# Optimization experiments

Measured on AMD Instinct MI355X. Metric: run time of the kernel, lower is better.

The kernel has to match this reference:

```python
import jax, jax.numpy as jnp
import numpy as np

B, S, HID = 4, 2048, 1024
NH, IM, E = 4, 2048, 4
EPS = 1e-6


def setup_inputs() -> dict:
    key = jax.random.key(0)
    ks = jax.random.split(key, 12)
    init = lambda k, shape: (jax.random.normal(k, shape, jnp.float32) * 0.02)
    return {
        "hidden_states": jax.random.normal(ks[0], (B, S, HID), jnp.float32),
        "ln1_w": jnp.ones((HID,), jnp.float32),
        "wq": init(ks[1], (HID, HID)),
        "wk": init(ks[2], (HID, HID)),
        "wv": init(ks[3], (HID, HID)),
        "wo": init(ks[4], (HID, HID)),
        "ln2_w": jnp.ones((HID,), jnp.float32),
        "router_w": init(ks[5], (HID, E)),
        "router_b": jnp.zeros((E,), jnp.float32),
        "gate_w": init(ks[6], (E, HID, IM)),
        "up_w": init(ks[7], (E, HID, IM)),
        "down_w": init(ks[8], (E, IM, HID)),
    }


def _rms(x, w):
    return w * (x * jax.lax.rsqrt(jnp.mean(x * x, axis=-1, keepdims=True) + EPS))


def reference(hidden_states, ln1_w, wq, wk, wv, wo, ln2_w,
              router_w, router_b, gate_w, up_w, down_w):
    b, s, h = hidden_states.shape
    nh, d = NH, h // NH

    # ---- attention block (elu+1 feature map, then full softmax) ----
    x = _rms(hidden_states, ln1_w)
    q = (x @ wq).reshape(b, s, nh, d).transpose(0, 2, 1, 3)  # [b,nh,s,d]
    k = (x @ wk).reshape(b, s, nh, d).transpose(0, 2, 1, 3)
    v = (x @ wv).reshape(b, s, nh, d).transpose(0, 2, 1, 3)
    q = jax.nn.elu(q) + 1.0
    k = jax.nn.elu(k) + 1.0
    scores = jnp.einsum('bhqd,bhkd->bhqk', q, k)
    attn = jax.nn.softmax(scores, axis=-1)  # dropout is identity at eval
    o = jnp.einsum('bhqk,bhkd->bhqd', attn, v)
    o = o.transpose(0, 2, 1, 3).reshape(b, s, h) @ wo
    h1 = hidden_states + o

    # ---- MoE block: router softmax, balance loss, dense expert loop ----
    x2 = _rms(h1, ln2_w)
    logits = x2 @ router_w + router_b            # [b,s,E]
    rw = jax.nn.softmax(logits, axis=-1)
    mean_routing = rw.mean(axis=0)               # mean over batch dim only, [s,E]
    balance_loss = jnp.mean((mean_routing - 1.0 / E) ** 2) * 0.01

    # source computes EVERY expert over all tokens, weighted by the FULL
    # softmax routing weight (top-k weights are computed but unused)
    moe_out = jnp.zeros_like(x2)
    for i in range(E):
        g = jax.nn.silu(x2 @ gate_w[i])
        u = x2 @ up_w[i]
        moe_out = moe_out + ((g * u) @ down_w[i]) * rw[..., i:i + 1]

    return h1 + moe_out, balance_loss
```

## Files before the change

kernel.cpp:

```cpp
#include <hip/hip_runtime.h>
#include <cstdint>
#include <cstddef>

#define B_    4
#define S_    2048
#define HID_  1024
#define NH_   4
#define HD_   256
#define IM_   2048
#define E_    4
#define M_    8192
#define NHG_  4

typedef __bf16 bf16x8 __attribute__((ext_vector_type(8)));
typedef float  f32x4  __attribute__((ext_vector_type(4)));

__device__ __forceinline__ unsigned short f32_to_bf16(float f) {
  unsigned int u = __float_as_uint(f);
  u += 0x7fffu + ((u >> 16) & 1u);
  return (unsigned short)(u >> 16);
}
__device__ __forceinline__ float bf16_to_f32(unsigned short s) {
  return __uint_as_float((unsigned int)s << 16);
}

__device__ __forceinline__ void gload16(const unsigned short* g, unsigned short* l) {
  __builtin_amdgcn_global_load_lds(
      (const __attribute__((address_space(1))) void*)g,
      (__attribute__((address_space(3))) void*)l, 16, 0, 0);
}

__device__ __forceinline__ void swizzle_xy(int& bx, int& by) {
  const int gx = gridDim.x, gy = gridDim.y;
  const int flat = blockIdx.x + blockIdx.y * gx;
  const int xcd = flat & 7, i = flat >> 3;
  const int rpx = gy >> 3;
  bx = i % gx;
  by = xcd * rpx + i / gx;
}

#define EPI_F32      0
#define EPI_ELU_BF16 1
#define EPI_VT       2
#define EPI_PV_O     3
#define EPI_WO       4
#define EPI_DOWN     5

struct EpiAux {
  float* c_f32;
  unsigned short* c_bf16;
  const float* add_src;
  float* out2;
  const float* rw;
  int expert;
  long long strideCz;
  int ldc;
};

template<int EPI>
__global__ __launch_bounds__(256) void gemm_bf16k(
    const unsigned short* __restrict__ A, int lda, long long sAo, long long sAi, int zbA,
    const unsigned short* __restrict__ B, int ldb, long long sBo, long long sBi, int zbB,
    int zshift, int zmask, int zbC, int K, EpiAux aux)
{
  __shared__ unsigned short As[2][128 * 32];
  __shared__ unsigned short Bs[2][128 * 32];

  const int t = threadIdx.x;
  int bx, by;
  swizzle_xy(bx, by);
  const int m0 = by * 128, n0 = bx * 128;
  const int z  = blockIdx.z;
  const int zA = z + zbA, zB = z + zbB, zC = z + zbC;
  const unsigned short* Ab = A + (long long)(zA >> zshift) * sAo + (long long)(zA & zmask) * sAi;
  const unsigned short* Bb = B + (long long)(zB >> zshift) * sBo + (long long)(zB & zmask) * sBi;

  const int lane = t & 63, wave = t >> 6;
  const int wm = (wave >> 1) * 64, wn = (wave & 1) * 64;
  const int lrow = lane & 15, quad = lane >> 4;

  f32x4 acc[4][4] = {};

  const int srow = lane >> 2;
  const int sko  = (lane & 3) * 8;
  const unsigned short* aRow0 = Ab + (long long)(m0 + wave * 16       + srow) * lda + sko;
  const unsigned short* aRow1 = Ab + (long long)(m0 + (wave + 4) * 16 + srow) * lda + sko;
  const unsigned short* bRow0 = Bb + (long long)(n0 + wave * 16       + srow) * ldb + sko;
  const unsigned short* bRow1 = Bb + (long long)(n0 + (wave + 4) * 16 + srow) * ldb + sko;
  const int dst0 = (wave * 16) * 32, dst1 = ((wave + 4) * 16) * 32;

  gload16(aRow0, &As[0][dst0]);
  gload16(aRow1, &As[0][dst1]);
  gload16(bRow0, &Bs[0][dst0]);
  gload16(bRow1, &Bs[0][dst1]);

  int cur = 0;
  for (int kk = 0; kk < K; kk += 32, cur ^= 1) {
    __syncthreads();
    if (kk + 32 < K) {
      const int nxt = cur ^ 1, k2 = kk + 32;
      gload16(aRow0 + k2, &As[nxt][dst0]);
      gload16(aRow1 + k2, &As[nxt][dst1]);
      gload16(bRow0 + k2, &Bs[nxt][dst0]);
      gload16(bRow1 + k2, &Bs[nxt][dst1]);
    }
    bf16x8 af[4], bfr[4];
    #pragma unroll
    for (int i = 0; i < 4; ++i) {
      af[i]  = *reinterpret_cast<const bf16x8*>(&As[cur][(wm + i * 16 + lrow) * 32 + quad * 8]);
      bfr[i] = *reinterpret_cast<const bf16x8*>(&Bs[cur][(wn + i * 16 + lrow) * 32 + quad * 8]);
    }
    #pragma unroll
    for (int i = 0; i < 4; ++i)
      #pragma unroll
      for (int j = 0; j < 4; ++j)
        acc[i][j] = __builtin_amdgcn_mfma_f32_16x16x32_bf16(af[i], bfr[j], acc[i][j], 0, 0, 0);
  }

  #pragma unroll
  for (int mi = 0; mi < 4; ++mi) {
    #pragma unroll
    for (int ni = 0; ni < 4; ++ni) {
      #pragma unroll
      for (int r = 0; r < 4; ++r) {
        const int gm = m0 + wm + mi * 16 + quad * 4 + r;
        const int gn = n0 + wn + ni * 16 + lrow;
        const float val = acc[mi][ni][r];
        if (EPI == EPI_F32) {
          aux.c_f32[(long long)zC * aux.strideCz + (long long)gm * aux.ldc + gn] = val;
        } else if (EPI == EPI_ELU_BF16) {
          const float e = val > 0.f ? val + 1.f : __expf(val);
          aux.c_bf16[(long long)gm * aux.ldc + gn] = f32_to_bf16(e);
        } else if (EPI == EPI_VT) {
          const int b = gm >> 11, s = gm & (S_ - 1);
          const int h = gn >> 8, d = gn & (HD_ - 1);
          aux.c_bf16[((long long)(b * NH_ + h) * HD_ + d) * S_ + s] = f32_to_bf16(val);
        } else if (EPI == EPI_PV_O) {
          const int b = zC >> 2, h = zC & (NH_ - 1);
          aux.c_bf16[((long long)(b * S_ + gm)) * HID_ + h * HD_ + gn] = f32_to_bf16(val);
        } else if (EPI == EPI_WO) {
          const long long idx = (long long)gm * HID_ + gn;
          aux.out2[idx] = val + aux.add_src[idx];
        } else if (EPI == EPI_DOWN) {
          const long long idx = (long long)gm * HID_ + gn;
          aux.out2[idx] += val * aux.rw[(long long)gm * E_ + aux.expert];
        }
      }
    }
  }
}

__global__ __launch_bounds__(256, 2) void gemm_gu_k(
    const unsigned short* __restrict__ A,
    const unsigned short* __restrict__ Bg,
    const unsigned short* __restrict__ Bu,
    unsigned short* __restrict__ gu)
{
  __shared__ unsigned short As[2][128 * 32];
  __shared__ unsigned short Bgs[2][128 * 32];
  __shared__ unsigned short Bus[2][128 * 32];

  const int t = threadIdx.x;
  int bx, by;
  swizzle_xy(bx, by);
  const int m0 = by * 128, n0 = bx * 128;

  const int lane = t & 63, wave = t >> 6;
  const int wm = (wave >> 1) * 64, wn = (wave & 1) * 64;
  const int lrow = lane & 15, quad = lane >> 4;

  f32x4 accg[4][4] = {}, accu[4][4] = {};

  const int srow = lane >> 2;
  const int sko  = (lane & 3) * 8;
  const unsigned short* aRow0 = A  + (long long)(m0 + wave * 16       + srow) * HID_ + sko;
  const unsigned short* aRow1 = A  + (long long)(m0 + (wave + 4) * 16 + srow) * HID_ + sko;
  const unsigned short* gRow0 = Bg + (long long)(n0 + wave * 16       + srow) * HID_ + sko;
  const unsigned short* gRow1 = Bg + (long long)(n0 + (wave + 4) * 16 + srow) * HID_ + sko;
  const unsigned short* uRow0 = Bu + (long long)(n0 + wave * 16       + srow) * HID_ + sko;
  const unsigned short* uRow1 = Bu + (long long)(n0 + (wave + 4) * 16 + srow) * HID_ + sko;
  const int dst0 = (wave * 16) * 32, dst1 = ((wave + 4) * 16) * 32;

  gload16(aRow0, &As[0][dst0]);
  gload16(aRow1, &As[0][dst1]);
  gload16(gRow0, &Bgs[0][dst0]);
  gload16(gRow1, &Bgs[0][dst1]);
  gload16(uRow0, &Bus[0][dst0]);
  gload16(uRow1, &Bus[0][dst1]);

  int cur = 0;
  for (int kk = 0; kk < HID_; kk += 32, cur ^= 1) {
    __syncthreads();
    if (kk + 32 < HID_) {
      const int nxt = cur ^ 1, k2 = kk + 32;
      gload16(aRow0 + k2, &As[nxt][dst0]);
      gload16(aRow1 + k2, &As[nxt][dst1]);
      gload16(gRow0 + k2, &Bgs[nxt][dst0]);
      gload16(gRow1 + k2, &Bgs[nxt][dst1]);
      gload16(uRow0 + k2, &Bus[nxt][dst0]);
      gload16(uRow1 + k2, &Bus[nxt][dst1]);
    }
    bf16x8 af[4], bg[4], bu[4];
    #pragma unroll
    for (int i = 0; i < 4; ++i) {
      af[i] = *reinterpret_cast<const bf16x8*>(&As[cur][(wm + i * 16 + lrow) * 32 + quad * 8]);
      bg[i] = *reinterpret_cast<const bf16x8*>(&Bgs[cur][(wn + i * 16 + lrow) * 32 + quad * 8]);
      bu[i] = *reinterpret_cast<const bf16x8*>(&Bus[cur][(wn + i * 16 + lrow) * 32 + quad * 8]);
    }
    #pragma unroll
    for (int i = 0; i < 4; ++i)
      #pragma unroll
      for (int j = 0; j < 4; ++j) {
        accg[i][j] = __builtin_amdgcn_mfma_f32_16x16x32_bf16(af[i], bg[j], accg[i][j], 0, 0, 0);
        accu[i][j] = __builtin_amdgcn_mfma_f32_16x16x32_bf16(af[i], bu[j], accu[i][j], 0, 0, 0);
      }
  }

  #pragma unroll
  for (int mi = 0; mi < 4; ++mi)
    #pragma unroll
    for (int ni = 0; ni < 4; ++ni)
      #pragma unroll
      for (int r = 0; r < 4; ++r) {
        const int gm = m0 + wm + mi * 16 + quad * 4 + r;
        const int gn = n0 + wn + ni * 16 + lrow;
        const float g = accg[mi][ni][r];
        const float u = accu[mi][ni][r];
        const float sg = g / (1.f + __expf(-g));
        gu[(long long)gm * IM_ + gn] = f32_to_bf16(sg * u);
      }
}

__global__ void transpose_cast_k(const float* __restrict__ in,
                                 unsigned short* __restrict__ out, int R, int C)
{
  __shared__ float tile[32][33];
  const long long bo = (long long)blockIdx.z * R * C;
  const int c0 = blockIdx.x * 32, r0 = blockIdx.y * 32;
  const int tx = threadIdx.x, ty = threadIdx.y;
  #pragma unroll
  for (int i = 0; i < 32; i += 8)
    tile[ty + i][tx] = in[bo + (long long)(r0 + ty + i) * C + c0 + tx];
  __syncthreads();
  #pragma unroll
  for (int i = 0; i < 32; i += 8)
    out[bo + (long long)(c0 + ty + i) * R + r0 + tx] = f32_to_bf16(tile[tx][ty + i]);
}

__global__ __launch_bounds__(256) void rmsnorm_cast_k(
    const float* __restrict__ x, const float* __restrict__ w,
    unsigned short* __restrict__ out)
{
  __shared__ float red[4];
  const int row = blockIdx.x, t = threadIdx.x;
  const float4 v = reinterpret_cast<const float4*>(x + (long long)row * HID_)[t];
  float ss = v.x * v.x + v.y * v.y + v.z * v.z + v.w * v.w;
  #pragma unroll
  for (int off = 32; off > 0; off >>= 1) ss += __shfl_down(ss, off, 64);
  if ((t & 63) == 0) red[t >> 6] = ss;
  __syncthreads();
  ss = red[0] + red[1] + red[2] + red[3];
  const float inv = rsqrtf(ss * (1.0f / HID_) + 1e-6f);
  const float4 wv = reinterpret_cast<const float4*>(w)[t];
  ushort4 o;
  o.x = f32_to_bf16(v.x * inv * wv.x);
  o.y = f32_to_bf16(v.y * inv * wv.y);
  o.z = f32_to_bf16(v.z * inv * wv.z);
  o.w = f32_to_bf16(v.w * inv * wv.w);
  reinterpret_cast<ushort4*>(out + (long long)row * HID_)[t] = o;
}

__global__ __launch_bounds__(256) void softmax_rows_k(float* __restrict__ scores)
{
  __shared__ float red[4];
  const long long rbase = ((long long)blockIdx.y * S_ + blockIdx.x) * S_;
  float* row = scores + rbase;
  const int t = threadIdx.x;
  float v[8];
  #pragma unroll
  for (int i = 0; i < 8; ++i) v[i] = row[t + i * 256];
  float m = v[0];
  #pragma unroll
  for (int i = 1; i < 8; ++i) m = fmaxf(m, v[i]);
  #pragma unroll
  for (int off = 32; off > 0; off >>= 1) m = fmaxf(m, __shfl_down(m, off, 64));
  if ((t & 63) == 0) red[t >> 6] = m;
  __syncthreads();
  m = fmaxf(fmaxf(red[0], red[1]), fmaxf(red[2], red[3]));
  __syncthreads();
  float s = 0.f;
  #pragma unroll
  for (int i = 0; i < 8; ++i) { v[i] = __expf(v[i] - m); s += v[i]; }
  #pragma unroll
  for (int off = 32; off > 0; off >>= 1) s += __shfl_down(s, off, 64);
  if ((t & 63) == 0) red[t >> 6] = s;
  __syncthreads();
  const float inv = 1.0f / (red[0] + red[1] + red[2] + red[3]);
  unsigned short* prow = reinterpret_cast<unsigned short*>(scores) + rbase * 2;
  #pragma unroll
  for (int i = 0; i < 8; ++i) prow[t + i * 256] = f32_to_bf16(v[i] * inv);
}

__global__ __launch_bounds__(256) void router_k(
    const float* __restrict__ h1, const float* __restrict__ ln2w,
    const float* __restrict__ rwgt, const float* __restrict__ rbias,
    float* __restrict__ rw)
{
  const int wv = threadIdx.x >> 6, lane = threadIdx.x & 63;
  const long long m = (long long)blockIdx.x * 4 + wv;
  const float* xr = h1 + m * HID_;
  float xv[16];
  float ss = 0.f;
  #pragma unroll
  for (int i = 0; i < 16; ++i) { xv[i] = xr[lane + i * 64]; ss += xv[i] * xv[i]; }
  #pragma unroll
  for (int off = 32; off > 0; off >>= 1) ss += __shfl_down(ss, off, 64);
  ss = __shfl(ss, 0, 64);
  const float inv = rsqrtf(ss * (1.0f / HID_) + 1e-6f);
  float l0 = 0, l1 = 0, l2 = 0, l3 = 0;
  #pragma unroll
  for (int i = 0; i < 16; ++i) {
    const int k = lane + i * 64;
    const float xn = xv[i] * inv * ln2w[k];
    const float4 wr = reinterpret_cast<const float4*>(rwgt)[k];
    l0 += xn * wr.x; l1 += xn * wr.y; l2 += xn * wr.z; l3 += xn * wr.w;
  }
  #pragma unroll
  for (int off = 32; off > 0; off >>= 1) {
    l0 += __shfl_down(l0, off, 64);
    l1 += __shfl_down(l1, off, 64);
    l2 += __shfl_down(l2, off, 64);
    l3 += __shfl_down(l3, off, 64);
  }
  if (lane == 0) {
    l0 += rbias[0]; l1 += rbias[1]; l2 += rbias[2]; l3 += rbias[3];
    const float mx = fmaxf(fmaxf(l0, l1), fmaxf(l2, l3));
    const float e0 = __expf(l0 - mx), e1 = __expf(l1 - mx);
    const float e2 = __expf(l2 - mx), e3 = __expf(l3 - mx);
    const float is = 1.0f / (e0 + e1 + e2 + e3);
    reinterpret_cast<float4*>(rw)[m] = make_float4(e0 * is, e1 * is, e2 * is, e3 * is);
  }
}

__global__ __launch_bounds__(256) void balance_k(const float* __restrict__ rw,
                                                 float* __restrict__ out_scalar)
{
  __shared__ float red[4];
  float acc = 0.f;
  for (int it = threadIdx.x; it < S_ * E_; it += 256) {
    const int s = it >> 2, e = it & 3;
    float mr = 0.f;
    #pragma unroll
    for (int b = 0; b < B_; ++b) mr += rw[((long long)b * S_ + s) * E_ + e];
    mr *= (1.0f / B_);
    const float d = mr - 1.0f / E_;
    acc += d * d;
  }
  #pragma unroll
  for (int off = 32; off > 0; off >>= 1) acc += __shfl_down(acc, off, 64);
  if ((threadIdx.x & 63) == 0) red[threadIdx.x >> 6] = acc;
  __syncthreads();
  if (threadIdx.x == 0)
    out_scalar[0] = (red[0] + red[1] + red[2] + red[3]) * (0.01f / (S_ * E_));
}

extern "C" void kernel_launch(void* const* d_in, const int* in_sizes, int n_in,
                              void* d_out, int out_size, void* d_ws, size_t ws_size,
                              hipStream_t stream)
{
  const float* hidden   = (const float*)d_in[0];
  const float* ln1w     = (const float*)d_in[1];
  const float* wq       = (const float*)d_in[2];
  const float* wk       = (const float*)d_in[3];
  const float* wv       = (const float*)d_in[4];
  const float* wo       = (const float*)d_in[5];
  const float* ln2w     = (const float*)d_in[6];
  const float* router_w = (const float*)d_in[7];
  const float* router_b = (const float*)d_in[8];
  const float* gate_w   = (const float*)d_in[9];
  const float* up_w     = (const float*)d_in[10];
  const float* down_w   = (const float*)d_in[11];
  float* out = (float*)d_out;

  char* ws = (char*)d_ws;
  size_t off = 0;
  auto carve = [&](size_t bytes) {
    off = (off + 255) & ~(size_t)255;
    char* p = ws + off;
    off += bytes;
    return p;
  };
  unsigned short* wqT   = (unsigned short*)carve((size_t)HID_ * HID_ * 2);
  unsigned short* wkT   = (unsigned short*)carve((size_t)HID_ * HID_ * 2);
  unsigned short* wvT   = (unsigned short*)carve((size_t)HID_ * HID_ * 2);
  unsigned short* woT   = (unsigned short*)carve((size_t)HID_ * HID_ * 2);
  unsigned short* x_bf  = (unsigned short*)carve((size_t)M_ * HID_ * 2);
  unsigned short* qb    = (unsigned short*)carve((size_t)M_ * HID_ * 2);
  unsigned short* kb    = (unsigned short*)carve((size_t)M_ * HID_ * 2);
  unsigned short* vT    = (unsigned short*)carve((size_t)M_ * HID_ * 2);
  float*          rwbuf = (float*)carve((size_t)M_ * E_ * 4);
  char*           ubase = carve((size_t)NHG_ * S_ * S_ * 4);
  float*          scores = (float*)ubase;
  unsigned short* gateT = (unsigned short*)(ubase);
  unsigned short* upT   = (unsigned short*)(ubase + (size_t)16 * 1024 * 1024);
  unsigned short* downT = (unsigned short*)(ubase + (size_t)32 * 1024 * 1024);
  unsigned short* o_bf  = x_bf;
  unsigned short* x2_bf = qb;
  unsigned short* gu    = kb;

  const dim3 blk256(256), blkT(32, 8);

  transpose_cast_k<<<dim3(32, 32, 1), blkT, 0, stream>>>(wq, wqT, HID_, HID_);
  transpose_cast_k<<<dim3(32, 32, 1), blkT, 0, stream>>>(wk, wkT, HID_, HID_);
  transpose_cast_k<<<dim3(32, 32, 1), blkT, 0, stream>>>(wv, wvT, HID_, HID_);
  transpose_cast_k<<<dim3(32, 32, 1), blkT, 0, stream>>>(wo, woT, HID_, HID_);

  rmsnorm_cast_k<<<M_, blk256, 0, stream>>>(hidden, ln1w, x_bf);

  {
    EpiAux a{}; a.c_bf16 = qb; a.ldc = HID_;
    gemm_bf16k<EPI_ELU_BF16><<<dim3(8, 64, 1), blk256, 0, stream>>>(
        x_bf, HID_, 0, 0, 0, wqT, HID_, 0, 0, 0, 0, 0, 0, HID_, a);
  }
  {
    EpiAux a{}; a.c_bf16 = kb; a.ldc = HID_;
    gemm_bf16k<EPI_ELU_BF16><<<dim3(8, 64, 1), blk256, 0, stream>>>(
        x_bf, HID_, 0, 0, 0, wkT, HID_, 0, 0, 0, 0, 0, 0, HID_, a);
  }
  {
    EpiAux a{}; a.c_bf16 = vT;
    gemm_bf16k<EPI_VT><<<dim3(8, 64, 1), blk256, 0, stream>>>(
        x_bf, HID_, 0, 0, 0, wvT, HID_, 0, 0, 0, 0, 0, 0, HID_, a);
  }

  for (int grp = 0; grp < 16 / NHG_; ++grp) {
    EpiAux as{}; as.c_f32 = scores; as.ldc = S_; as.strideCz = (long long)S_ * S_;
    gemm_bf16k<EPI_F32><<<dim3(16, 16, NHG_), blk256, 0, stream>>>(
        qb, HID_, (long long)S_ * HID_, HD_, grp * NHG_,
        kb, HID_, (long long)S_ * HID_, HD_, grp * NHG_,
        2, 3, 0, HD_, as);
    softmax_rows_k<<<dim3(S_, NHG_, 1), blk256, 0, stream>>>(scores);
    EpiAux ap{}; ap.c_bf16 = o_bf;
    gemm_bf16k<EPI_PV_O><<<dim3(2, 16, NHG_), blk256, 0, stream>>>(
        (const unsigned short*)scores, 2 * S_, (long long)S_ * 2 * S_, 0, 0,
        vT, S_, (long long)HD_ * S_, 0, grp * NHG_,
        0, 0, grp * NHG_, S_, ap);
  }

  transpose_cast_k<<<dim3(64, 32, E_), blkT, 0, stream>>>(gate_w, gateT, HID_, IM_);
  transpose_cast_k<<<dim3(64, 32, E_), blkT, 0, stream>>>(up_w,   upT,   HID_, IM_);
  transpose_cast_k<<<dim3(32, 64, E_), blkT, 0, stream>>>(down_w, downT, IM_, HID_);

  {
    EpiAux a{}; a.add_src = hidden; a.out2 = out;
    gemm_bf16k<EPI_WO><<<dim3(8, 64, 1), blk256, 0, stream>>>(
        o_bf, HID_, 0, 0, 0, woT, HID_, 0, 0, 0, 0, 0, 0, HID_, a);
  }

  rmsnorm_cast_k<<<M_, blk256, 0, stream>>>(out, ln2w, x2_bf);
  router_k<<<M_ / 4, blk256, 0, stream>>>(out, ln2w, router_w, router_b, rwbuf);
  balance_k<<<1, blk256, 0, stream>>>(rwbuf, out + (size_t)M_ * HID_);

  for (int i = 0; i < E_; ++i) {
    gemm_gu_k<<<dim3(16, 64, 1), blk256, 0, stream>>>(
        x2_bf, gateT + (size_t)i * IM_ * HID_, upT + (size_t)i * IM_ * HID_, gu);
    EpiAux ad{}; ad.out2 = out; ad.rw = rwbuf; ad.expert = i;
    gemm_bf16k<EPI_DOWN><<<dim3(8, 64, 1), blk256, 0, stream>>>(
        gu, IM_, 0, 0, 0, downT + (size_t)i * HID_ * IM_, IM_, 0, 0, 0,
        0, 0, 0, IM_, ad);
  }
}
```

Baseline: 1.195 ms.

## Pair MoE experts in gate/up and down GEMMs, fuse Q/K projections and transposes

Fuses the Q and K projections into one dual-output GEMM sharing the A tile. The routing weight now multiplies gu in the gate/up epilogue instead of the down epilogue. Two experts run per launch: gate/up over a z=2 grid into two gu buffers, then one down GEMM that accumulates both experts' K loops before a single read-modify-write of out. This halves the output RMW traffic and the launch count. The weight transposes are batched into fewer launches, at the cost of a larger workspace (extra gu buffer), higher LDS use in the down kernel, and a fallback path when the workspace is too small.

Result: slower. 1.390 ms (+16.4%).

```diff
diff --git a/kernel.cpp b/kernel.cpp
--- a/kernel.cpp
+++ b/kernel.cpp
@@ -20,9 +20,6 @@
   u += 0x7fffu + ((u >> 16) & 1u);
   return (unsigned short)(u >> 16);
 }
-__device__ __forceinline__ float bf16_to_f32(unsigned short s) {
-  return __uint_as_float((unsigned int)s << 16);
-}
 
 __device__ __forceinline__ void gload16(const unsigned short* g, unsigned short* l) {
   __builtin_amdgcn_global_load_lds(
@@ -40,7 +37,6 @@
 }
 
 #define EPI_F32      0
-#define EPI_ELU_BF16 1
 #define EPI_VT       2
 #define EPI_PV_O     3
 #define EPI_WO       4
@@ -51,8 +47,6 @@
   unsigned short* c_bf16;
   const float* add_src;
   float* out2;
-  const float* rw;
-  int expert;
   long long strideCz;
   int ldc;
 };
@@ -128,9 +122,6 @@
         const float val = acc[mi][ni][r];
         if (EPI == EPI_F32) {
           aux.c_f32[(long long)zC * aux.strideCz + (long long)gm * aux.ldc + gn] = val;
-        } else if (EPI == EPI_ELU_BF16) {
-          const float e = val > 0.f ? val + 1.f : __expf(val);
-          aux.c_bf16[(long long)gm * aux.ldc + gn] = f32_to_bf16(e);
         } else if (EPI == EPI_VT) {
           const int b = gm >> 11, s = gm & (S_ - 1);
           const int h = gn >> 8, d = gn & (HD_ - 1);
@@ -143,50 +134,59 @@
           aux.out2[idx] = val + aux.add_src[idx];
         } else if (EPI == EPI_DOWN) {
           const long long idx = (long long)gm * HID_ + gn;
-          aux.out2[idx] += val * aux.rw[(long long)gm * E_ + aux.expert];
+          aux.out2[idx] += val;
         }
       }
     }
   }
 }
 
-__global__ __launch_bounds__(256, 2) void gemm_gu_k(
+#define EPI2_QK 0
+#define EPI2_GU 1
+
+template<int EPI2>
+__global__ __launch_bounds__(256) void gemm_dual_k(
     const unsigned short* __restrict__ A,
-    const unsigned short* __restrict__ Bg,
-    const unsigned short* __restrict__ Bu,
-    unsigned short* __restrict__ gu)
+    const unsigned short* __restrict__ B0b,
+    const unsigned short* __restrict__ B1b,
+    long long sB, int zb,
+    unsigned short* __restrict__ out0, unsigned short* __restrict__ out1,
+    const float* __restrict__ rw)
 {
   __shared__ unsigned short As[2][128 * 32];
-  __shared__ unsigned short Bgs[2][128 * 32];
-  __shared__ unsigned short Bus[2][128 * 32];
+  __shared__ unsigned short B0s[2][128 * 32];
+  __shared__ unsigned short B1s[2][128 * 32];
 
   const int t = threadIdx.x;
   int bx, by;
   swizzle_xy(bx, by);
   const int m0 = by * 128, n0 = bx * 128;
+  const int z = blockIdx.z;
+  const unsigned short* Bb0 = B0b + (long long)z * sB;
+  const unsigned short* Bb1 = B1b + (long long)z * sB;
 
   const int lane = t & 63, wave = t >> 6;
   const int wm = (wave >> 1) * 64, wn = (wave & 1) * 64;
   const int lrow = lane & 15, quad = lane >> 4;
 
-  f32x4 accg[4][4] = {}, accu[4][4] = {};
+  f32x4 acc0[4][4] = {}, acc1[4][4] = {};
 
   const int srow = lane >> 2;
   const int sko  = (lane & 3) * 8;
-  const unsigned short* aRow0 = A  + (long long)(m0 + wave * 16       + srow) * HID_ + sko;
-  const unsigned short* aRow1 = A  + (long long)(m0 + (wave + 4) * 16 + srow) * HID_ + sko;
-  const unsigned short* gRow0 = Bg + (long long)(n0 + wave * 16       + srow) * HID_ + sko;
-  const unsigned short* gRow1 = Bg + (long long)(n0 + (wave + 4) * 16 + srow) * HID_ + sko;
-  const unsigned short* uRow0 = Bu + (long long)(n0 + wave * 16       + srow) * HID_ + sko;
-  const unsigned short* uRow1 = Bu + (long long)(n0 + (wave + 4) * 16 + srow) * HID_ + sko;
+  const unsigned short* aRow0 = A   + (long long)(m0 + wave * 16       + srow) * HID_ + sko;
+  const unsigned short* aRow1 = A   + (long long)(m0 + (wave + 4) * 16 + srow) * HID_ + sko;
+  const unsigned short* gRow0 = Bb0 + (long long)(n0 + wave * 16       + srow) * HID_ + sko;
+  const unsigned short* gRow1 = Bb0 + (long long)(n0 + (wave + 4) * 16 + srow) * HID_ + sko;
+  const unsigned short* uRow0 = Bb1 + (long long)(n0 + wave * 16       + srow) * HID_ + sko;
+  const unsigned short* uRow1 = Bb1 + (long long)(n0 + (wave + 4) * 16 + srow) * HID_ + sko;
   const int dst0 = (wave * 16) * 32, dst1 = ((wave + 4) * 16) * 32;
 
   gload16(aRow0, &As[0][dst0]);
   gload16(aRow1, &As[0][dst1]);
-  gload16(gRow0, &Bgs[0][dst0]);
-  gload16(gRow1, &Bgs[0][dst1]);
-  gload16(uRow0, &Bus[0][dst0]);
-  gload16(uRow1, &Bus[0][dst1]);
+  gload16(gRow0, &B0s[0][dst0]);
+  gload16(gRow1, &B0s[0][dst1]);
+  gload16(uRow0, &B1s[0][dst0]);
+  gload16(uRow1, &B1s[0][dst1]);
 
   int cur = 0;
   for (int kk = 0; kk < HID_; kk += 32, cur ^= 1) {
@@ -195,24 +195,127 @@
       const int nxt = cur ^ 1, k2 = kk + 32;
       gload16(aRow0 + k2, &As[nxt][dst0]);
       gload16(aRow1 + k2, &As[nxt][dst1]);
-      gload16(gRow0 + k2, &Bgs[nxt][dst0]);
-      gload16(gRow1 + k2, &Bgs[nxt][dst1]);
-      gload16(uRow0 + k2, &Bus[nxt][dst0]);
-      gload16(uRow1 + k2, &Bus[nxt][dst1]);
-    }
-    bf16x8 af[4], bg[4], bu[4];
+      gload16(gRow0 + k2, &B0s[nxt][dst0]);
+      gload16(gRow1 + k2, &B0s[nxt][dst1]);
+      gload16(uRow0 + k2, &B1s[nxt][dst0]);
+      gload16(uRow1 + k2, &B1s[nxt][dst1]);
+    }
+    bf16x8 af[4], b0[4], b1[4];
     #pragma unroll
     for (int i = 0; i < 4; ++i) {
       af[i] = *reinterpret_cast<const bf16x8*>(&As[cur][(wm + i * 16 + lrow) * 32 + quad * 8]);
-      bg[i] = *reinterpret_cast<const bf16x8*>(&Bgs[cur][(wn + i * 16 + lrow) * 32 + quad * 8]);
-      bu[i] = *reinterpret_cast<const bf16x8*>(&Bus[cur][(wn + i * 16 + lrow) * 32 + quad * 8]);
+      b0[i] = *reinterpret_cast<const bf16x8*>(&B0s[cur][(wn + i * 16 + lrow) * 32 + quad * 8]);
+      b1[i] = *reinterpret_cast<const bf16x8*>(&B1s[cur][(wn + i * 16 + lrow) * 32 + quad * 8]);
     }
     #pragma unroll
     for (int i = 0; i < 4; ++i)
       #pragma unroll
       for (int j = 0; j < 4; ++j) {
-        accg[i][j] = __builtin_amdgcn_mfma_f32_16x16x32_bf16(af[i], bg[j], accg[i][j], 0, 0, 0);
-        accu[i][j] = __builtin_amdgcn_mfma_f32_16x16x32_bf16(af[i], bu[j], accu[i][j], 0, 0, 0);
+        acc0[i][j] = __builtin_amdgcn_mfma_f32_16x16x32_bf16(af[i], b0[j], acc0[i][j], 0, 0, 0);
+        acc1[i][j] = __builtin_amdgcn_mfma_f32_16x16x32_bf16(af[i], b1[j], acc1[i][j], 0, 0, 0);
+      }
+  }
+
+  unsigned short* dsel = (z == 0) ? out0 : out1;
+  const int expert = zb + z;
+
+  #pragma unroll
+  for (int mi = 0; mi < 4; ++mi)
+    #pragma unroll
+    for (int r = 0; r < 4; ++r) {
+      const int gm = m0 + wm + mi * 16 + quad * 4 + r;
+      float rwv = 0.f;
+      if (EPI2 == EPI2_GU) rwv = rw[(long long)gm * E_ + expert];
+      #pragma unroll
+      for (int ni = 0; ni < 4; ++ni) {
+        const int gn = n0 + wn + ni * 16 + lrow;
+        const float v0 = acc0[mi][ni][r];
+        const float v1 = acc1[mi][ni][r];
+        if (EPI2 == EPI2_QK) {
+          const float eq = v0 > 0.f ? v0 + 1.f : __expf(v0);
+          const float ek = v1 > 0.f ? v1 + 1.f : __expf(v1);
+          out0[(long long)gm * HID_ + gn] = f32_to_bf16(eq);
+          out1[(long long)gm * HID_ + gn] = f32_to_bf16(ek);
+        } else {
+          const float sg = v0 / (1.f + __expf(-v0));
+          dsel[(long long)gm * IM_ + gn] = f32_to_bf16(sg * v1 * rwv);
+        }
+      }
+    }
+}
+
+__global__ __launch_bounds__(256) void gemm_down2_k(
+    const unsigned short* __restrict__ A0,
+    const unsigned short* __restrict__ A1,
+    const unsigned short* __restrict__ B0,
+    const unsigned short* __restrict__ B1,
+    float* __restrict__ out)
+{
+  __shared__ unsigned short A0s[2][128 * 32];
+  __shared__ unsigned short A1s[2][128 * 32];
+  __shared__ unsigned short B0s[2][128 * 32];
+  __shared__ unsigned short B1s[2][128 * 32];
+
+  const int t = threadIdx.x;
+  int bx, by;
+  swizzle_xy(bx, by);
+  const int m0 = by * 128, n0 = bx * 128;
+
+  const int lane = t & 63, wave = t >> 6;
+  const int wm = (wave >> 1) * 64, wn = (wave & 1) * 64;
+  const int lrow = lane & 15, quad = lane >> 4;
+
+  f32x4 acc[4][4] = {};
+
+  const int srow = lane >> 2;
+  const int sko  = (lane & 3) * 8;
+  const unsigned short* a0r0 = A0 + (long long)(m0 + wave * 16       + srow) * IM_ + sko;
+  const unsigned short* a0r1 = A0 + (long long)(m0 + (wave + 4) * 16 + srow) * IM_ + sko;
+  const unsigned short* a1r0 = A1 + (long long)(m0 + wave * 16       + srow) * IM_ + sko;
+  const unsigned short* a1r1 = A1 + (long long)(m0 + (wave + 4) * 16 + srow) * IM_ + sko;
+  const unsigned short* b0r0 = B0 + (long long)(n0 + wave * 16       + srow) * IM_ + sko;
+  const unsigned short* b0r1 = B0 + (long long)(n0 + (wave + 4) * 16 + srow) * IM_ + sko;
+  const unsigned short* b1r0 = B1 + (long long)(n0 + wave * 16       + srow) * IM_ + sko;
+  const unsigned short* b1r1 = B1 + (long long)(n0 + (wave + 4) * 16 + srow) * IM_ + sko;
+  const int dst0 = (wave * 16) * 32, dst1 = ((wave + 4) * 16) * 32;
+
+  gload16(a0r0, &A0s[0][dst0]);
+  gload16(a0r1, &A0s[0][dst1]);
+  gload16(a1r0, &A1s[0][dst0]);
+  gload16(a1r1, &A1s[0][dst1]);
+  gload16(b0r0, &B0s[0][dst0]);
+  gload16(b0r1, &B0s[0][dst1]);
+  gload16(b1r0, &B1s[0][dst0]);
+  gload16(b1r1, &B1s[0][dst1]);
+
+  int cur = 0;
+  for (int kk = 0; kk < IM_; kk += 32, cur ^= 1) {
+    __syncthreads();
+    if (kk + 32 < IM_) {
+      const int nxt = cur ^ 1, k2 = kk + 32;
+      gload16(a0r0 + k2, &A0s[nxt][dst0]);
+      gload16(a0r1 + k2, &A0s[nxt][dst1]);
+      gload16(a1r0 + k2, &A1s[nxt][dst0]);
+      gload16(a1r1 + k2, &A1s[nxt][dst1]);
+      gload16(b0r0 + k2, &B0s[nxt][dst0]);
+      gload16(b0r1 + k2, &B0s[nxt][dst1]);
+      gload16(b1r0 + k2, &B1s[nxt][dst0]);
+      gload16(b1r1 + k2, &B1s[nxt][dst1]);
+    }
+    bf16x8 a0f[4], a1f[4], b0f[4], b1f[4];
+    #pragma unroll
+    for (int i = 0; i < 4; ++i) {
+      a0f[i] = *reinterpret_cast<const bf16x8*>(&A0s[cur][(wm + i * 16 + lrow) * 32 + quad * 8]);
+      a1f[i] = *reinterpret_cast<const bf16x8*>(&A1s[cur][(wm + i * 16 + lrow) * 32 + quad * 8]);
+      b0f[i] = *reinterpret_cast<const bf16x8*>(&B0s[cur][(wn + i * 16 + lrow) * 32 + quad * 8]);
+      b1f[i] = *reinterpret_cast<const bf16x8*>(&B1s[cur][(wn + i * 16 + lrow) * 32 + quad * 8]);
+    }
+    #pragma unroll
+    for (int i = 0; i < 4; ++i)
+      #pragma unroll
+      for (int j = 0; j < 4; ++j) {
+        acc[i][j] = __builtin_amdgcn_mfma_f32_16x16x32_bf16(a0f[i], b0f[j], acc[i][j], 0, 0, 0);
+        acc[i][j] = __builtin_amdgcn_mfma_f32_16x16x32_bf16(a1f[i], b1f[j], acc[i][j], 0, 0, 0);
       }
   }
 
@@ -224,11 +327,49 @@
       for (int r = 0; r < 4; ++r) {
         const int gm = m0 + wm + mi * 16 + quad * 4 + r;
         const int gn = n0 + wn + ni * 16 + lrow;
-        const float g = accg[mi][ni][r];
-        const float u = accu[mi][ni][r];
-        const float sg = g / (1.f + __expf(-g));
-        gu[(long long)gm * IM_ + gn] = f32_to_bf16(sg * u);
+        out[(long long)gm * HID_ + gn] += acc[mi][ni][r];
       }
+}
+
+__global__ void transpose_cast4_k(const float* s0, const float* s1,
+                                  const float* s2, const float* s3,
+                                  unsigned short* __restrict__ out, int R, int C)
+{
+  __shared__ float tile[32][33];
+  const int z = blockIdx.z;
+  const float* in = (z == 0) ? s0 : (z == 1) ? s1 : (z == 2) ? s2 : s3;
+  unsigned short* o = out + (long long)z * R * C;
+  const int c0 = blockIdx.x * 32, r0 = blockIdx.y * 32;
+  const int tx = threadIdx.x, ty = threadIdx.y;
+  #pragma unroll
+  for (int i = 0; i < 32; i += 8)
+    tile[ty + i][tx] = in[(long long)(r0 + ty + i) * C + c0 + tx];
+  __syncthreads();
+  #pragma unroll
+  for (int i = 0; i < 32; i += 8)
+    o[(long long)(c0 + ty + i) * R + r0 + tx] = f32_to_bf16(tile[tx][ty + i]);
+}
+
+__global__ void transpose_cast2x4_k(const float* __restrict__ sA,
+                                    const float* __restrict__ sB,
+                                    unsigned short* __restrict__ dA,
+                                    unsigned short* __restrict__ dB,
+                                    int R, int C)
+{
+  __shared__ float tile[32][33];
+  const int z = blockIdx.z;
+  const long long eo = (long long)(z & 3) * R * C;
+  const float* in = ((z < 4) ? sA : sB) + eo;
+  unsigned short* o = ((z < 4) ? dA : dB) + eo;
+  const int c0 = blockIdx.x * 32, r0 = blockIdx.y * 32;
+  const int tx = threadIdx.x, ty = threadIdx.y;
+  #pragma unroll
+  for (int i = 0; i < 32; i += 8)
+    tile[ty + i][tx] = in[(long long)(r0 + ty + i) * C + c0 + tx];
+  __syncthreads();
+  #pragma unroll
+  for (int i = 0; i < 32; i += 8)
+    o[(long long)(c0 + ty + i) * R + r0 + tx] = f32_to_bf16(tile[tx][ty + i]);
 }
 
 __global__ void transpose_cast_k(const float* __restrict__ in,
@@ -400,33 +541,26 @@
   unsigned short* vT    = (unsigned short*)carve((size_t)M_ * HID_ * 2);
   float*          rwbuf = (float*)carve((size_t)M_ * E_ * 4);
   char*           ubase = carve((size_t)NHG_ * S_ * S_ * 4);
+  const size_t base_bytes = off;
   float*          scores = (float*)ubase;
   unsigned short* gateT = (unsigned short*)(ubase);
   unsigned short* upT   = (unsigned short*)(ubase + (size_t)16 * 1024 * 1024);
   unsigned short* downT = (unsigned short*)(ubase + (size_t)32 * 1024 * 1024);
   unsigned short* o_bf  = x_bf;
   unsigned short* x2_bf = qb;
-  unsigned short* gu    = kb;
+  unsigned short* gu0   = kb;
+  unsigned short* gu1   = (unsigned short*)carve((size_t)M_ * IM_ * 2);
+  const bool paired = (ws_size >= off);
+  (void)base_bytes;
 
   const dim3 blk256(256), blkT(32, 8);
 
-  transpose_cast_k<<<dim3(32, 32, 1), blkT, 0, stream>>>(wq, wqT, HID_, HID_);
-  transpose_cast_k<<<dim3(32, 32, 1), blkT, 0, stream>>>(wk, wkT, HID_, HID_);
-  transpose_cast_k<<<dim3(32, 32, 1), blkT, 0, stream>>>(wv, wvT, HID_, HID_);
-  transpose_cast_k<<<dim3(32, 32, 1), blkT, 0, stream>>>(wo, woT, HID_, HID_);
+  transpose_cast4_k<<<dim3(32, 32, 4), blkT, 0, stream>>>(wq, wk, wv, wo, wqT, HID_, HID_);
 
   rmsnorm_cast_k<<<M_, blk256, 0, stream>>>(hidden, ln1w, x_bf);
 
-  {
-    EpiAux a{}; a.c_bf16 = qb; a.ldc = HID_;
-    gemm_bf16k<EPI_ELU_BF16><<<dim3(8, 64, 1), blk256, 0, stream>>>(
-        x_bf, HID_, 0, 0, 0, wqT, HID_, 0, 0, 0, 0, 0, 0, HID_, a);
-  }
-  {
-    EpiAux a{}; a.c_bf16 = kb; a.ldc = HID_;
-    gemm_bf16k<EPI_ELU_BF16><<<dim3(8, 64, 1), blk256, 0, stream>>>(
-        x_bf, HID_, 0, 0, 0, wkT, HID_, 0, 0, 0, 0, 0, 0, HID_, a);
-  }
+  gemm_dual_k<EPI2_QK><<<dim3(8, 64, 1), blk256, 0, stream>>>(
+      x_bf, wqT, wkT, 0, 0, qb, kb, nullptr);
   {
     EpiAux a{}; a.c_bf16 = vT;
     gemm_bf16k<EPI_VT><<<dim3(8, 64, 1), blk256, 0, stream>>>(
@@ -447,8 +581,8 @@
         0, 0, grp * NHG_, S_, ap);
   }
 
-  transpose_cast_k<<<dim3(64, 32, E_), blkT, 0, stream>>>(gate_w, gateT, HID_, IM_);
-  transpose_cast_k<<<dim3(64, 32, E_), blkT, 0, stream>>>(up_w,   upT,   HID_, IM_);
+  transpose_cast2x4_k<<<dim3(64, 32, 8), blkT, 0, stream>>>(
+      gate_w, up_w, gateT, upT, HID_, IM_);
   transpose_cast_k<<<dim3(32, 64, E_), blkT, 0, stream>>>(down_w, downT, IM_, HID_);
 
   {
@@ -461,12 +595,25 @@
   router_k<<<M_ / 4, blk256, 0, stream>>>(out, ln2w, router_w, router_b, rwbuf);
   balance_k<<<1, blk256, 0, stream>>>(rwbuf, out + (size_t)M_ * HID_);
 
-  for (int i = 0; i < E_; ++i) {
-    gemm_gu_k<<<dim3(16, 64, 1), blk256, 0, stream>>>(
-        x2_bf, gateT + (size_t)i * IM_ * HID_, upT + (size_t)i * IM_ * HID_, gu);
-    EpiAux ad{}; ad.out2 = out; ad.rw = rwbuf; ad.expert = i;
-    gemm_bf16k<EPI_DOWN><<<dim3(8, 64, 1), blk256, 0, stream>>>(
-        gu, IM_, 0, 0, 0, downT + (size_t)i * HID_ * IM_, IM_, 0, 0, 0,
-        0, 0, 0, IM_, ad);
-  }
-}
+  const size_t wsz = (size_t)IM_ * HID_;
+  if (paired) {
+    for (int p = 0; p < 2; ++p) {
+      const int e0 = 2 * p;
+      gemm_dual_k<EPI2_GU><<<dim3(16, 64, 2), blk256, 0, stream>>>(
+          x2_bf, gateT + (size_t)e0 * wsz, upT + (size_t)e0 * wsz,
+          (long long)wsz, e0, gu0, gu1, rwbuf);
+      gemm_down2_k<<<dim3(8, 64, 1), blk256, 0, stream>>>(
+          gu0, gu1, downT + (size_t)e0 * wsz, downT + (size_t)(e0 + 1) * wsz, out);
+    }
+  } else {
+    for (int i = 0; i < E_; ++i) {
+      gemm_dual_k<EPI2_GU><<<dim3(16, 64, 1), blk256, 0, stream>>>(
+          x2_bf, gateT + (size_t)i * wsz, upT + (size_t)i * wsz,
+          0, i, gu0, gu0, rwbuf);
+      EpiAux ad{}; ad.out2 = out;
+      gemm_bf16k<EPI_DOWN><<<dim3(8, 64, 1), blk256, 0, stream>>>(
+          gu0, IM_, 0, 0, 0, downT + (size_t)i * wsz, IM_, 0, 0, 0,
+          0, 0, 0, IM_, ad);
+    }
+  }
+}
```
